# Kernel optimization log

Measured on AMD Instinct MI355X. Metric: run time of the kernel, lower is better.

Reference implementation:

```python
import jax, jax.numpy as jnp
import numpy as np

NEG = -1e30  # log-space 'zero' (safe substitute for -inf)
EPS = 1e-7   # keras.backend.epsilon(), used by ctc_batch_cost


def _ctc_forward(logp, z, allow2):
    """CTC negative log-likelihood via the forward DP in log space.
    logp:   [B, T, C] log-probabilities
    z:      [B, S] extended label sequence (blanks interleaved), S = 2L+1
    allow2: [B, S] bool, whether the skip transition (s-2 -> s) is legal
    Returns [B, 1] loss (matches keras ctc_batch_cost output shape).
    """
    B, T, C = logp.shape
    S = z.shape[1]
    # Gather per-timestep log-probs of extended labels: [B, T, S] -> [T, B, S]
    b_idx = jnp.arange(B)[:, None, None]
    t_idx = jnp.arange(T)[None, :, None]
    lp_z = jnp.transpose(logp[b_idx, t_idx, z[:, None, :]], (1, 0, 2))

    s_idx = jnp.arange(S)[None, :]
    alpha0 = jnp.where(s_idx < 2, lp_z[0], NEG)  # paths may start at blank or first label

    def step(alpha, lp_t):
        a1 = jnp.concatenate([jnp.full((B, 1), NEG, alpha.dtype), alpha[:, :-1]], axis=1)
        a2 = jnp.concatenate([jnp.full((B, 2), NEG, alpha.dtype), alpha[:, :-2]], axis=1)
        a2 = jnp.where(allow2, a2, NEG)
        m = jnp.maximum(alpha, jnp.maximum(a1, a2))
        lse = m + jnp.log(jnp.exp(alpha - m) + jnp.exp(a1 - m) + jnp.exp(a2 - m))
        return lp_t + lse, None

    alphaT, _ = jax.lax.scan(step, alpha0, lp_z[1:])
    # Paths end at last blank (S-1) or last label (S-2)
    last, last2 = alphaT[:, -1], alphaT[:, -2]
    m = jnp.maximum(last, last2)
    ll = m + jnp.log(jnp.exp(last - m) + jnp.exp(last2 - m))
    return -ll[:, None]


def setup_inputs() -> dict:
    key = jax.random.key(0)
    k1, k2 = jax.random.split(key)
    B, T, C, L = 32, 2048, 256, 256
    # ctc_batch_cost expects post-softmax probabilities
    y_pred = jax.nn.softmax(jax.random.normal(k1, (B, T, C), jnp.float32), axis=-1)
    y_true = jax.random.randint(k2, (B, L), 0, C - 1)  # blank = C-1 excluded from labels
    return {"y_true": y_true, "y_pred": y_pred}


def reference(y_true, y_pred):
    B, T, C = y_pred.shape
    blank = C - 1
    L = y_true.shape[1]
    S = 2 * L + 1
    labels = y_true.astype(jnp.int32)
    # Extended label sequence: blank, l0, blank, l1, ..., blank
    z = jnp.full((B, S), blank, jnp.int32).at[:, 1::2].set(labels)
    z_m2 = jnp.concatenate([jnp.full((B, 2), -1, jnp.int32), z[:, :-2]], axis=1)
    allow2 = (z != blank) & (z != z_m2)
    logp = jnp.log(y_pred + EPS)
    return _ctc_forward(logp, z, allow2)
```

## Files before the change

kernel.cpp:

```cpp
#include <hip/hip_runtime.h>

#define TT   2048
#define CC   256
#define LL   256
#define SS   513
#define TM   1023
#define EPSF (1e-7f)
#define LN2F (0.69314718055994531f)
#define DPTH 8
#define RBTH 64
#define NCH  127
#define EMINI (-2000000000)

#if __has_builtin(__builtin_amdgcn_frexp_expf)
#define FREXP_EXP __builtin_amdgcn_frexp_expf
#else
static __device__ __forceinline__ int FREXP_EXP(float x){ int e; frexpf(x,&e); return e; }
#endif
#if __has_builtin(__builtin_amdgcn_ldexpf)
#define LDEXP __builtin_amdgcn_ldexpf
#else
#define LDEXP ldexpf
#endif


__launch_bounds__(128, 1)
__global__ void ctc_mim_kernel(const int* __restrict__ y_true,
                               const float* __restrict__ y_pred,
                               float* __restrict__ out)
{
    __shared__ float cw[SS];
    __shared__ int   ew[64];

    const int tid   = threadIdx.x;
    const int w     = tid >> 6;
    const int lane  = tid & 63;
    const int b     = blockIdx.x;
    const int blank = CC - 1;

    const int*   lab  = y_true + b * LL;
    const float* base = y_pred + (size_t)b * TT * CC;

    int   col[4];
    float kup[4];
    float kdn[4];
    #pragma unroll
    for (int i = 0; i < 4; ++i) {
        const int li = 4 * lane + i;
        const int z  = lab[li];
        col[i] = z;
        const int zm = (li >= 1) ? lab[li - 1] : -1;
        kup[i] = (z != zm) ? 1.0f : 0.0f;
        kdn[i] = (li <= 254 && lab[li + 1] != z) ? 1.0f : 0.0f;
    }

    float f[9];
    #pragma unroll
    for (int j = 0; j < 9; ++j) f[j] = 0.0f;
    int  e = 0;
    bool lzero;

    if (w == 0) {
        if (lane == 0) {
            f[0] = base[blank]  + EPSF;
            f[1] = base[col[0]] + EPSF;
        }
        lzero = (lane != 0);
    } else {
        if (lane == 63) {
            const float* rT = base + (size_t)(TT - 1) * CC;
            f[7] = rT[col[3]] + EPSF;
            f[8] = rT[blank]  + EPSF;
        }
        lzero = (lane != 63);
    }

    float pfb[DPTH];
    float pfl[DPTH][4];
    #pragma unroll
    for (int k = 0; k < DPTH; ++k) {
        const int r = (w == 0) ? (1 + k) : (TT - 2 - k);
        const float* rp = base + (size_t)r * CC;
        pfb[k] = rp[blank];
        #pragma unroll
        for (int i = 0; i < 4; ++i) pfl[k][i] = rp[col[i]];
    }

    auto renorm = [&]() {
        float m = fmaxf(fmaxf(fmaxf(f[0], f[1]), fmaxf(f[2], f[3])),
                        fmaxf(fmaxf(f[4], f[5]), fmaxf(f[6], fmaxf(f[7], f[8]))));
        const int em = FREXP_EXP(m);
        #pragma unroll
        for (int j = 0; j < 9; ++j) f[j] = LDEXP(f[j], -em);
        e += em;
    };

    auto fwd_step = [&](float pb, float p0, float p1, float p2, float p3) {
        float u7 = __shfl_up(f[7], 1);
        int   ue = __shfl_up(e, 1);
        if (lane == 0) { u7 = 0.0f; ue = e; }
        int dlt = ue - e;
        const bool rb = lzero || (dlt >= RBTH);
        if (__ballot(rb)) {
            const int sh = rb ? -dlt : 0;
            #pragma unroll
            for (int j = 0; j < 9; ++j) f[j] = LDEXP(f[j], sh);
            e   = rb ? ue : e;
            dlt = rb ? 0  : dlt;
            lzero = lzero && (u7 == 0.0f);
        }
        const float bf = LDEXP(u7, dlt);
        const float n0 = (f[0] + bf) * pb;
        const float n1 = (f[1] + f[0] + bf   * kup[0]) * p0;
        const float n2 = (f[2] + f[1]) * pb;
        const float n3 = (f[3] + f[2] + f[1] * kup[1]) * p1;
        const float n4 = (f[4] + f[3]) * pb;
        const float n5 = (f[5] + f[4] + f[3] * kup[2]) * p2;
        const float n6 = (f[6] + f[5]) * pb;
        const float n7 = (f[7] + f[6] + f[5] * kup[3]) * p3;
        const float n8 = (f[8] + f[7]) * pb;
        f[0]=n0; f[1]=n1; f[2]=n2; f[3]=n3; f[4]=n4;
        f[5]=n5; f[6]=n6; f[7]=n7; f[8]=n8;
    };

    auto bwd_step = [&](float pb, float p0, float p1, float p2, float p3) {
        float d1 = __shfl_down(f[1], 1);
        int   de = __shfl_down(e, 1);
        if (lane == 63) { d1 = 0.0f; de = e; }
        int dlt = de - e;
        const bool rb = lzero || (dlt >= RBTH);
        if (__ballot(rb)) {
            const int sh = rb ? -dlt : 0;
            #pragma unroll
            for (int j = 0; j < 9; ++j) f[j] = LDEXP(f[j], sh);
            e   = rb ? de : e;
            dlt = rb ? 0  : dlt;
            lzero = lzero && (d1 == 0.0f);
        }
        const float bf = LDEXP(d1, dlt);
        const float n0 = (f[0] + f[1]) * pb;
        const float n1 = (f[1] + f[2] + f[3] * kdn[0]) * p0;
        const float n2 = (f[2] + f[3]) * pb;
        const float n3 = (f[3] + f[4] + f[5] * kdn[1]) * p1;
        const float n4 = (f[4] + f[5]) * pb;
        const float n5 = (f[5] + f[6] + f[7] * kdn[2]) * p2;
        const float n6 = (f[6] + f[7]) * pb;
        const float n7 = (f[7] + f[8] + bf   * kdn[3]) * p3;
        const float n8 = (f[8] + bf) * pb;
        f[0]=n0; f[1]=n1; f[2]=n2; f[3]=n3; f[4]=n4;
        f[5]=n5; f[6]=n6; f[7]=n7; f[8]=n8;
    };

    if (w == 0) {
        for (int c = 0; c < NCH; ++c) {
            #pragma unroll
            for (int k = 0; k < DPTH; ++k) {
                const float pb = pfb[k]    + EPSF;
                const float p0 = pfl[k][0] + EPSF;
                const float p1 = pfl[k][1] + EPSF;
                const float p2 = pfl[k][2] + EPSF;
                const float p3 = pfl[k][3] + EPSF;
                int tp = 1 + c * DPTH + k + DPTH; if (tp > TM) tp = TM;
                const float* rp = base + (size_t)tp * CC;
                pfb[k] = rp[blank];
                #pragma unroll
                for (int i = 0; i < 4; ++i) pfl[k][i] = rp[col[i]];
                fwd_step(pb, p0, p1, p2, p3);
                if (k == 3 || k == 7) renorm();
            }
        }
        #pragma unroll
        for (int k = 0; k < 7; ++k) {
            fwd_step(pfb[k] + EPSF, pfl[k][0] + EPSF, pfl[k][1] + EPSF,
                     pfl[k][2] + EPSF, pfl[k][3] + EPSF);
            if (k == 3) renorm();
        }
    } else {
        for (int c = 0; c < NCH; ++c) {
            #pragma unroll
            for (int k = 0; k < DPTH; ++k) {
                const float pb = pfb[k]    + EPSF;
                const float p0 = pfl[k][0] + EPSF;
                const float p1 = pfl[k][1] + EPSF;
                const float p2 = pfl[k][2] + EPSF;
                const float p3 = pfl[k][3] + EPSF;
                int tp = (TT - 2) - (c * DPTH + k) - DPTH; if (tp < TM + 1) tp = TM + 1;
                const float* rp = base + (size_t)tp * CC;
                pfb[k] = rp[blank];
                #pragma unroll
                for (int i = 0; i < 4; ++i) pfl[k][i] = rp[col[i]];
                bwd_step(pb, p0, p1, p2, p3);
                if (k == 3 || k == 7) renorm();
            }
        }
        #pragma unroll
        for (int k = 0; k < 7; ++k) {
            bwd_step(pfb[k] + EPSF, pfl[k][0] + EPSF, pfl[k][1] + EPSF,
                     pfl[k][2] + EPSF, pfl[k][3] + EPSF);
            if (k == 3) renorm();
        }

        float d1 = __shfl_down(f[1], 1);
        int   de = __shfl_down(e, 1);
        if (lane == 63) { d1 = 0.0f; de = e; }
        int dlt = de - e;
        if (dlt >= RBTH) {
            #pragma unroll
            for (int j = 0; j < 9; ++j) f[j] = LDEXP(f[j], -dlt);
            e = de; dlt = 0;
        }
        const float bf = LDEXP(d1, dlt);
        float cb[9];
        cb[0] = f[0] + f[1];
        cb[1] = f[1] + f[2] + f[3] * kdn[0];
        cb[2] = f[2] + f[3];
        cb[3] = f[3] + f[4] + f[5] * kdn[1];
        cb[4] = f[4] + f[5];
        cb[5] = f[5] + f[6] + f[7] * kdn[2];
        cb[6] = f[6] + f[7];
        cb[7] = f[7] + f[8] + bf   * kdn[3];
        cb[8] = f[8] + bf;

        #pragma unroll
        for (int j = 0; j < 8; ++j) cw[8 * lane + j] = cb[j];
        if (lane == 63) cw[512] = cb[8];
        ew[lane] = e;
    }

    __syncthreads();

    if (w == 0) {
        float part = 0.0f;
        #pragma unroll
        for (int j = 0; j < 8; ++j) part += f[j] * cw[8 * lane + j];
        if (lane == 63) part += f[8] * cw[512];
        int   ep = (part > 0.0f) ? (e + ew[lane]) : EMINI;
        float m  = part;
        #pragma unroll
        for (int d = 1; d < 64; d <<= 1) {
            const float mo = __shfl_xor(m, d);
            const int   eo = __shfl_xor(ep, d);
            const int   E  = max(ep, eo);
            m  = LDEXP(m, ep - E) + LDEXP(mo, eo - E);
            ep = E;
        }
        if (lane == 0)
            out[b] = -LN2F * ((float)ep + __builtin_amdgcn_logf(m));
    }
}

extern "C" void kernel_launch(void* const* d_in, const int* in_sizes, int n_in,
                              void* d_out, int out_size, void* d_ws, size_t ws_size,
                              hipStream_t stream)
{
    const int*   y_true = (const int*)d_in[0];
    const float* y_pred = (const float*)d_in[1];
    float*       out    = (float*)d_out;
    const int B = in_sizes[0] / LL;
    ctc_mim_kernel<<<B, 128, 0, stream>>>(y_true, y_pred, out);
}
```

Baseline: 195.7 us.

## Stage probability rows into an LDS ring via async global-to-LDS loads

Replaces the per-lane scattered global gathers of five probabilities per timestep with coalesced 16-byte-per-lane global_load_lds copies of whole rows into a 10-slot shared-memory ring. The five values are then read from LDS and double-buffered in registers, with explicit vmcnt waits keeping 8 rows in flight. The goal is to hide global latency on the serial DP chain and avoid uncoalesced gathers. The cost is more LDS traffic, a dependence on hand-written waitcnt ordering without an explicit LDS fence, and a rewritten loop tail.

Result: slower. 286.5 us (+46.4%).

```diff
diff --git a/kernel.cpp b/kernel.cpp
--- a/kernel.cpp
+++ b/kernel.cpp
@@ -7,9 +7,9 @@
 #define TM   1023
 #define EPSF (1e-7f)
 #define LN2F (0.69314718055994531f)
-#define DPTH 8
+#define RING 10
+#define RD   8
 #define RBTH 64
-#define NCH  127
 #define EMINI (-2000000000)
 
 #if __has_builtin(__builtin_amdgcn_frexp_expf)
@@ -23,12 +23,21 @@
 #define LDEXP ldexpf
 #endif
 
+__device__ __forceinline__ void stage16(const float* g, float* l)
+{
+    __builtin_amdgcn_global_load_lds(
+        (const __attribute__((address_space(1))) unsigned int*)g,
+        (__attribute__((address_space(3))) unsigned int*)l,
+        16, 0, 0);
+}
+
 
 __launch_bounds__(128, 1)
 __global__ void ctc_mim_kernel(const int* __restrict__ y_true,
                                const float* __restrict__ y_pred,
                                float* __restrict__ out)
 {
+    __shared__ float ring[2][RING][CC];
     __shared__ float cw[SS];
     __shared__ int   ew[64];
 
@@ -73,17 +82,6 @@
             f[8] = rT[blank]  + EPSF;
         }
         lzero = (lane != 63);
-    }
-
-    float pfb[DPTH];
-    float pfl[DPTH][4];
-    #pragma unroll
-    for (int k = 0; k < DPTH; ++k) {
-        const int r = (w == 0) ? (1 + k) : (TT - 2 - k);
-        const float* rp = base + (size_t)r * CC;
-        pfb[k] = rp[blank];
-        #pragma unroll
-        for (int i = 0; i < 4; ++i) pfl[k][i] = rp[col[i]];
     }
 
     auto renorm = [&]() {
@@ -151,53 +149,80 @@
         f[5]=n5; f[6]=n6; f[7]=n7; f[8]=n8;
     };
 
+#define LDPV(PV, SLOT) do {                                   \
+        PV[0] = ring[w][(SLOT)][col[0]] + EPSF;               \
+        PV[1] = ring[w][(SLOT)][col[1]] + EPSF;               \
+        PV[2] = ring[w][(SLOT)][col[2]] + EPSF;               \
+        PV[3] = ring[w][(SLOT)][col[3]] + EPSF;               \
+        PV[4] = ring[w][(SLOT)][CC - 1] + EPSF;               \
+    } while (0)
+
+#define VMWAIT(N) do {                                        \
+        asm volatile("s_waitcnt vmcnt(" #N ")" ::: "memory"); \
+        __builtin_amdgcn_sched_barrier(0);                    \
+    } while (0)
+
+    float pvA[5], pvB[5];
+
+    #pragma unroll
+    for (int j = 0; j < RD; ++j) {
+        const int r = (w == 0) ? (1 + j) : (TT - 2 - j);
+        stage16(base + (size_t)r * CC + 4 * lane, &ring[w][j][0]);
+    }
+    VMWAIT(7);
+    LDPV(pvA, 0);
+
     if (w == 0) {
-        for (int c = 0; c < NCH; ++c) {
-            #pragma unroll
-            for (int k = 0; k < DPTH; ++k) {
-                const float pb = pfb[k]    + EPSF;
-                const float p0 = pfl[k][0] + EPSF;
-                const float p1 = pfl[k][1] + EPSF;
-                const float p2 = pfl[k][2] + EPSF;
-                const float p3 = pfl[k][3] + EPSF;
-                int tp = 1 + c * DPTH + k + DPTH; if (tp > TM) tp = TM;
-                const float* rp = base + (size_t)tp * CC;
-                pfb[k] = rp[blank];
-                #pragma unroll
-                for (int i = 0; i < 4; ++i) pfl[k][i] = rp[col[i]];
-                fwd_step(pb, p0, p1, p2, p3);
+        for (int c = 0; c < 102; ++c) {
+            const int tb = 1 + c * 10;
+            #pragma unroll
+            for (int k = 0; k < 10; ++k) {
+                VMWAIT(6);
+                if ((k & 1) == 0) LDPV(pvB, (k + 1) % RING);
+                else              LDPV(pvA, (k + 1) % RING);
+                int sr = tb + k + RD; if (sr > TM) sr = TM;
+                stage16(base + (size_t)sr * CC + 4 * lane,
+                        &ring[w][(k + RD) % RING][0]);
+                if ((k & 1) == 0) fwd_step(pvA[4], pvA[0], pvA[1], pvA[2], pvA[3]);
+                else              fwd_step(pvB[4], pvB[0], pvB[1], pvB[2], pvB[3]);
                 if (k == 3 || k == 7) renorm();
             }
         }
         #pragma unroll
-        for (int k = 0; k < 7; ++k) {
-            fwd_step(pfb[k] + EPSF, pfl[k][0] + EPSF, pfl[k][1] + EPSF,
-                     pfl[k][2] + EPSF, pfl[k][3] + EPSF);
-            if (k == 3) renorm();
+        for (int k = 0; k < 3; ++k) {
+            VMWAIT(6);
+            if ((k & 1) == 0) LDPV(pvB, (k + 1) % RING);
+            else              LDPV(pvA, (k + 1) % RING);
+            stage16(base + (size_t)TM * CC + 4 * lane,
+                    &ring[w][(k + RD) % RING][0]);
+            if ((k & 1) == 0) fwd_step(pvA[4], pvA[0], pvA[1], pvA[2], pvA[3]);
+            else              fwd_step(pvB[4], pvB[0], pvB[1], pvB[2], pvB[3]);
         }
     } else {
-        for (int c = 0; c < NCH; ++c) {
-            #pragma unroll
-            for (int k = 0; k < DPTH; ++k) {
-                const float pb = pfb[k]    + EPSF;
-                const float p0 = pfl[k][0] + EPSF;
-                const float p1 = pfl[k][1] + EPSF;
-                const float p2 = pfl[k][2] + EPSF;
-                const float p3 = pfl[k][3] + EPSF;
-                int tp = (TT - 2) - (c * DPTH + k) - DPTH; if (tp < TM + 1) tp = TM + 1;
-                const float* rp = base + (size_t)tp * CC;
-                pfb[k] = rp[blank];
-                #pragma unroll
-                for (int i = 0; i < 4; ++i) pfl[k][i] = rp[col[i]];
-                bwd_step(pb, p0, p1, p2, p3);
+        for (int c = 0; c < 102; ++c) {
+            const int ib = c * 10;
+            #pragma unroll
+            for (int k = 0; k < 10; ++k) {
+                VMWAIT(6);
+                if ((k & 1) == 0) LDPV(pvB, (k + 1) % RING);
+                else              LDPV(pvA, (k + 1) % RING);
+                int sr = (TT - 2) - (ib + k + RD); if (sr < TM + 1) sr = TM + 1;
+                stage16(base + (size_t)sr * CC + 4 * lane,
+                        &ring[w][(k + RD) % RING][0]);
+                if ((k & 1) == 0) bwd_step(pvA[4], pvA[0], pvA[1], pvA[2], pvA[3]);
+                else              bwd_step(pvB[4], pvB[0], pvB[1], pvB[2], pvB[3]);
                 if (k == 3 || k == 7) renorm();
             }
         }
         #pragma unroll
-        for (int k = 0; k < 7; ++k) {
-            bwd_step(pfb[k] + EPSF, pfl[k][0] + EPSF, pfl[k][1] + EPSF,
-                     pfl[k][2] + EPSF, pfl[k][3] + EPSF);
-            if (k == 3) renorm();
+        for (int k = 0; k < 3; ++k) {
+            VMWAIT(6);
+            if ((k & 1) == 0) LDPV(pvB, (k + 1) % RING);
+            else              LDPV(pvA, (k + 1) % RING);
+            stage16(base + (size_t)(TM + 1) * CC + 4 * lane,
+                    &ring[w][(k + RD) % RING][0]);
+            if ((k & 1) == 0) bwd_step(pvA[4], pvA[0], pvA[1], pvA[2], pvA[3]);
+            else              bwd_step(pvB[4], pvB[0], pvB[1], pvB[2], pvB[3]);
         }
 
         float d1 = __shfl_down(f[1], 1);
```

## Pre-gather label probabilities into compact workspace before the recurrence kernel

Applied to the files above, without the earlier changes.

A separate, highly parallel kernel gathers per-timestep probabilities of each label and of the blank, with epsilon already added, into a contiguous workspace row of stride 260. The serial forward/backward kernel then reads one float4 plus one scalar per lane per step, replacing five scattered gathers. This is meant to take random-access gather latency off the latency-bound recurrence. The cost is an extra launch and writing then re-reading about 67MB of workspace. A fallback kernel identical to the old code runs when the workspace is too small.

Measured after the change: 205.1 us. 4.8% more time.

```diff
diff --git a/kernel.cpp b/kernel.cpp
--- a/kernel.cpp
+++ b/kernel.cpp
@@ -11,11 +11,12 @@
 #define RBTH 64
 #define NCH  127
 #define EMINI (-2000000000)
+#define GSTR 260
 
 #if __has_builtin(__builtin_amdgcn_frexp_expf)
 #define FREXP_EXP __builtin_amdgcn_frexp_expf
 #else
-static __device__ __forceinline__ int FREXP_EXP(float x){ int e; frexpf(x,&e); return e; }
+static __device__ __forceinline__ int FREXP_EXP(float x){ int e; return (frexpf(x,&e), e); }
 #endif
 #if __has_builtin(__builtin_amdgcn_ldexpf)
 #define LDEXP __builtin_amdgcn_ldexpf
@@ -23,11 +24,31 @@
 #define LDEXP ldexpf
 #endif
 
+__launch_bounds__(256, 4)
+__global__ void ctc_gather_kernel(const int* __restrict__ y_true,
+                                  const float* __restrict__ y_pred,
+                                  float* __restrict__ gat)
+{
+    const int b   = blockIdx.x;
+    const int i   = threadIdx.x;
+    const int col = y_true[b * LL + i];
+    const float* rp = y_pred + (size_t)b * TT * CC;
+    float*       gp = gat    + (size_t)b * TT * GSTR;
+    const int tch = TT / gridDim.y;
+    const int t0  = blockIdx.y * tch;
+    #pragma unroll 4
+    for (int t = t0; t < t0 + tch; ++t) {
+        gp[(size_t)t * GSTR + i] = rp[(size_t)t * CC + col] + EPSF;
+        if (i == 255)
+            gp[(size_t)t * GSTR + 256] = rp[(size_t)t * CC + (CC - 1)] + EPSF;
+    }
+}
 
 __launch_bounds__(128, 1)
-__global__ void ctc_mim_kernel(const int* __restrict__ y_true,
-                               const float* __restrict__ y_pred,
-                               float* __restrict__ out)
+__global__ void ctc_fast_kernel(const int* __restrict__ y_true,
+                                const float* __restrict__ y_pred,
+                                const float* __restrict__ gat,
+                                float* __restrict__ out)
 {
     __shared__ float cw[SS];
     __shared__ int   ew[64];
@@ -38,17 +59,17 @@
     const int b     = blockIdx.x;
     const int blank = CC - 1;
 
-    const int*   lab  = y_true + b * LL;
-    const float* base = y_pred + (size_t)b * TT * CC;
-
-    int   col[4];
+    const int*   lab   = y_true + b * LL;
+    const float* base  = y_pred + (size_t)b * TT * CC;
+    const float* gbase = gat    + (size_t)b * TT * GSTR;
+
+    int   col0 = lab[4 * lane];
     float kup[4];
     float kdn[4];
     #pragma unroll
     for (int i = 0; i < 4; ++i) {
         const int li = 4 * lane + i;
         const int z  = lab[li];
-        col[i] = z;
         const int zm = (li >= 1) ? lab[li - 1] : -1;
         kup[i] = (z != zm) ? 1.0f : 0.0f;
         kdn[i] = (li <= 254 && lab[li + 1] != z) ? 1.0f : 0.0f;
@@ -62,28 +83,27 @@
 
     if (w == 0) {
         if (lane == 0) {
-            f[0] = base[blank]  + EPSF;
-            f[1] = base[col[0]] + EPSF;
+            f[0] = base[blank] + EPSF;
+            f[1] = base[col0]  + EPSF;
         }
         lzero = (lane != 0);
     } else {
         if (lane == 63) {
             const float* rT = base + (size_t)(TT - 1) * CC;
-            f[7] = rT[col[3]] + EPSF;
-            f[8] = rT[blank]  + EPSF;
+            f[7] = rT[lab[255]] + EPSF;
+            f[8] = rT[blank]    + EPSF;
         }
         lzero = (lane != 63);
     }
 
-    float pfb[DPTH];
-    float pfl[DPTH][4];
+    float4 pf[DPTH];
+    float  pbf[DPTH];
     #pragma unroll
     for (int k = 0; k < DPTH; ++k) {
         const int r = (w == 0) ? (1 + k) : (TT - 2 - k);
-        const float* rp = base + (size_t)r * CC;
-        pfb[k] = rp[blank];
-        #pragma unroll
-        for (int i = 0; i < 4; ++i) pfl[k][i] = rp[col[i]];
+        const float* rp = gbase + (size_t)r * GSTR;
+        pf[k]  = *(const float4*)(rp + 4 * lane);
+        pbf[k] = rp[256];
     }
 
     auto renorm = [&]() {
@@ -155,48 +175,41 @@
         for (int c = 0; c < NCH; ++c) {
             #pragma unroll
             for (int k = 0; k < DPTH; ++k) {
-                const float pb = pfb[k]    + EPSF;
-                const float p0 = pfl[k][0] + EPSF;
-                const float p1 = pfl[k][1] + EPSF;
-                const float p2 = pfl[k][2] + EPSF;
-                const float p3 = pfl[k][3] + EPSF;
+                const float pb = pbf[k];
+                const float p0 = pf[k].x, p1 = pf[k].y,
+                            p2 = pf[k].z, p3 = pf[k].w;
                 int tp = 1 + c * DPTH + k + DPTH; if (tp > TM) tp = TM;
-                const float* rp = base + (size_t)tp * CC;
-                pfb[k] = rp[blank];
-                #pragma unroll
-                for (int i = 0; i < 4; ++i) pfl[k][i] = rp[col[i]];
+                const float* rp = gbase + (size_t)tp * GSTR;
+                pf[k]  = *(const float4*)(rp + 4 * lane);
+                pbf[k] = rp[256];
                 fwd_step(pb, p0, p1, p2, p3);
                 if (k == 3 || k == 7) renorm();
             }
         }
         #pragma unroll
         for (int k = 0; k < 7; ++k) {
-            fwd_step(pfb[k] + EPSF, pfl[k][0] + EPSF, pfl[k][1] + EPSF,
-                     pfl[k][2] + EPSF, pfl[k][3] + EPSF);
+            fwd_step(pbf[k], pf[k].x, pf[k].y, pf[k].z, pf[k].w);
             if (k == 3) renorm();
         }
     } else {
         for (int c = 0; c < NCH; ++c) {
             #pragma unroll
             for (int k = 0; k < DPTH; ++k) {
-                const float pb = pfb[k]    + EPSF;
-                const float p0 = pfl[k][0] + EPSF;
-                const float p1 = pfl[k][1] + EPSF;
-                const float p2 = pfl[k][2] + EPSF;
-                const float p3 = pfl[k][3] + EPSF;
-                int tp = (TT - 2) - (c * DPTH + k) - DPTH; if (tp < TM + 1) tp = TM + 1;
-                const float* rp = base + (size_t)tp * CC;
-                pfb[k] = rp[blank];
-                #pragma unroll
-                for (int i = 0; i < 4; ++i) pfl[k][i] = rp[col[i]];
+                const float pb = pbf[k];
+                const float p0 = pf[k].x, p1 = pf[k].y,
+                            p2 = pf[k].z, p3 = pf[k].w;
+                int tp = (TT - 2) - (c * DPTH + k) - DPTH;
+                if (tp < TM + 1) tp = TM + 1;
+                const float* rp = gbase + (size_t)tp * GSTR;
+                pf[k]  = *(const float4*)(rp + 4 * lane);
+                pbf[k] = rp[256];
                 bwd_step(pb, p0, p1, p2, p3);
                 if (k == 3 || k == 7) renorm();
             }
         }
         #pragma unroll
         for (int k = 0; k < 7; ++k) {
-            bwd_step(pfb[k] + EPSF, pfl[k][0] + EPSF, pfl[k][1] + EPSF,
-                     pfl[k][2] + EPSF, pfl[k][3] + EPSF);
+            bwd_step(pbf[k], pf[k].x, pf[k].y, pf[k].z, pf[k].w);
             if (k == 3) renorm();
         }
 
@@ -240,7 +253,217 @@
         for (int d = 1; d < 64; d <<= 1) {
             const float mo = __shfl_xor(m, d);
             const int   eo = __shfl_xor(ep, d);
-            const int   E  = max(ep, eo);
+            const int   E  = ep > eo ? ep : eo;
+            m  = LDEXP(m, ep - E) + LDEXP(mo, eo - E);
+            ep = E;
+        }
+        if (lane == 0)
+            out[b] = -LN2F * ((float)ep + __builtin_amdgcn_logf(m));
+    }
+}
+
+__launch_bounds__(128, 1)
+__global__ void ctc_fb_kernel(const int* __restrict__ y_true,
+                              const float* __restrict__ y_pred,
+                              float* __restrict__ out)
+{
+    __shared__ float cw[SS];
+    __shared__ int   ew[64];
+
+    const int tid   = threadIdx.x;
+    const int w     = tid >> 6;
+    const int lane  = tid & 63;
+    const int b     = blockIdx.x;
+    const int blank = CC - 1;
+
+    const int*   lab  = y_true + b * LL;
+    const float* base = y_pred + (size_t)b * TT * CC;
+
+    int   col[4];
+    float kup[4], kdn[4];
+    #pragma unroll
+    for (int i = 0; i < 4; ++i) {
+        const int li = 4 * lane + i;
+        const int z  = lab[li];
+        col[i] = z;
+        const int zm = (li >= 1) ? lab[li - 1] : -1;
+        kup[i] = (z != zm) ? 1.0f : 0.0f;
+        kdn[i] = (li <= 254 && lab[li + 1] != z) ? 1.0f : 0.0f;
+    }
+
+    float f[9];
+    #pragma unroll
+    for (int j = 0; j < 9; ++j) f[j] = 0.0f;
+    int  e = 0;
+    bool lzero;
+
+    if (w == 0) {
+        if (lane == 0) { f[0] = base[blank] + EPSF; f[1] = base[col[0]] + EPSF; }
+        lzero = (lane != 0);
+    } else {
+        if (lane == 63) {
+            const float* rT = base + (size_t)(TT - 1) * CC;
+            f[7] = rT[col[3]] + EPSF; f[8] = rT[blank] + EPSF;
+        }
+        lzero = (lane != 63);
+    }
+
+    float pfb[DPTH]; float pfl[DPTH][4];
+    #pragma unroll
+    for (int k = 0; k < DPTH; ++k) {
+        const int r = (w == 0) ? (1 + k) : (TT - 2 - k);
+        const float* rp = base + (size_t)r * CC;
+        pfb[k] = rp[blank];
+        #pragma unroll
+        for (int i = 0; i < 4; ++i) pfl[k][i] = rp[col[i]];
+    }
+
+    auto renorm = [&]() {
+        float m = fmaxf(fmaxf(fmaxf(f[0], f[1]), fmaxf(f[2], f[3])),
+                        fmaxf(fmaxf(f[4], f[5]), fmaxf(f[6], fmaxf(f[7], f[8]))));
+        const int em = FREXP_EXP(m);
+        #pragma unroll
+        for (int j = 0; j < 9; ++j) f[j] = LDEXP(f[j], -em);
+        e += em;
+    };
+    auto fwd_step = [&](float pb, float p0, float p1, float p2, float p3) {
+        float u7 = __shfl_up(f[7], 1);
+        int   ue = __shfl_up(e, 1);
+        if (lane == 0) { u7 = 0.0f; ue = e; }
+        int dlt = ue - e;
+        const bool rb = lzero || (dlt >= RBTH);
+        if (__ballot(rb)) {
+            const int sh = rb ? -dlt : 0;
+            #pragma unroll
+            for (int j = 0; j < 9; ++j) f[j] = LDEXP(f[j], sh);
+            e = rb ? ue : e; dlt = rb ? 0 : dlt;
+            lzero = lzero && (u7 == 0.0f);
+        }
+        const float bf = LDEXP(u7, dlt);
+        const float n0 = (f[0] + bf) * pb;
+        const float n1 = (f[1] + f[0] + bf   * kup[0]) * p0;
+        const float n2 = (f[2] + f[1]) * pb;
+        const float n3 = (f[3] + f[2] + f[1] * kup[1]) * p1;
+        const float n4 = (f[4] + f[3]) * pb;
+        const float n5 = (f[5] + f[4] + f[3] * kup[2]) * p2;
+        const float n6 = (f[6] + f[5]) * pb;
+        const float n7 = (f[7] + f[6] + f[5] * kup[3]) * p3;
+        const float n8 = (f[8] + f[7]) * pb;
+        f[0]=n0; f[1]=n1; f[2]=n2; f[3]=n3; f[4]=n4;
+        f[5]=n5; f[6]=n6; f[7]=n7; f[8]=n8;
+    };
+    auto bwd_step = [&](float pb, float p0, float p1, float p2, float p3) {
+        float d1 = __shfl_down(f[1], 1);
+        int   de = __shfl_down(e, 1);
+        if (lane == 63) { d1 = 0.0f; de = e; }
+        int dlt = de - e;
+        const bool rb = lzero || (dlt >= RBTH);
+        if (__ballot(rb)) {
+            const int sh = rb ? -dlt : 0;
+            #pragma unroll
+            for (int j = 0; j < 9; ++j) f[j] = LDEXP(f[j], sh);
+            e = rb ? de : e; dlt = rb ? 0 : dlt;
+            lzero = lzero && (d1 == 0.0f);
+        }
+        const float bf = LDEXP(d1, dlt);
+        const float n0 = (f[0] + f[1]) * pb;
+        const float n1 = (f[1] + f[2] + f[3] * kdn[0]) * p0;
+        const float n2 = (f[2] + f[3]) * pb;
+        const float n3 = (f[3] + f[4] + f[5] * kdn[1]) * p1;
+        const float n4 = (f[4] + f[5]) * pb;
+        const float n5 = (f[5] + f[6] + f[7] * kdn[2]) * p2;
+        const float n6 = (f[6] + f[7]) * pb;
+        const float n7 = (f[7] + f[8] + bf   * kdn[3]) * p3;
+        const float n8 = (f[8] + bf) * pb;
+        f[0]=n0; f[1]=n1; f[2]=n2; f[3]=n3; f[4]=n4;
+        f[5]=n5; f[6]=n6; f[7]=n7; f[8]=n8;
+    };
+
+    if (w == 0) {
+        for (int c = 0; c < NCH; ++c) {
+            #pragma unroll
+            for (int k = 0; k < DPTH; ++k) {
+                const float pb = pfb[k] + EPSF;
+                const float p0 = pfl[k][0] + EPSF, p1 = pfl[k][1] + EPSF;
+                const float p2 = pfl[k][2] + EPSF, p3 = pfl[k][3] + EPSF;
+                int tp = 1 + c * DPTH + k + DPTH; if (tp > TM) tp = TM;
+                const float* rp = base + (size_t)tp * CC;
+                pfb[k] = rp[blank];
+                #pragma unroll
+                for (int i = 0; i < 4; ++i) pfl[k][i] = rp[col[i]];
+                fwd_step(pb, p0, p1, p2, p3);
+                if (k == 3 || k == 7) renorm();
+            }
+        }
+        #pragma unroll
+        for (int k = 0; k < 7; ++k) {
+            fwd_step(pfb[k] + EPSF, pfl[k][0] + EPSF, pfl[k][1] + EPSF,
+                     pfl[k][2] + EPSF, pfl[k][3] + EPSF);
+            if (k == 3) renorm();
+        }
+    } else {
+        for (int c = 0; c < NCH; ++c) {
+            #pragma unroll
+            for (int k = 0; k < DPTH; ++k) {
+                const float pb = pfb[k] + EPSF;
+                const float p0 = pfl[k][0] + EPSF, p1 = pfl[k][1] + EPSF;
+                const float p2 = pfl[k][2] + EPSF, p3 = pfl[k][3] + EPSF;
+                int tp = (TT - 2) - (c * DPTH + k) - DPTH; if (tp < TM + 1) tp = TM + 1;
+                const float* rp = base + (size_t)tp * CC;
+                pfb[k] = rp[blank];
+                #pragma unroll
+                for (int i = 0; i < 4; ++i) pfl[k][i] = rp[col[i]];
+                bwd_step(pb, p0, p1, p2, p3);
+                if (k == 3 || k == 7) renorm();
+            }
+        }
+        #pragma unroll
+        for (int k = 0; k < 7; ++k) {
+            bwd_step(pfb[k] + EPSF, pfl[k][0] + EPSF, pfl[k][1] + EPSF,
+                     pfl[k][2] + EPSF, pfl[k][3] + EPSF);
+            if (k == 3) renorm();
+        }
+
+        float d1 = __shfl_down(f[1], 1);
+        int   de = __shfl_down(e, 1);
+        if (lane == 63) { d1 = 0.0f; de = e; }
+        int dlt = de - e;
+        if (dlt >= RBTH) {
+            #pragma unroll
+            for (int j = 0; j < 9; ++j) f[j] = LDEXP(f[j], -dlt);
+            e = de; dlt = 0;
+        }
+        const float bf = LDEXP(d1, dlt);
+        float cb[9];
+        cb[0] = f[0] + f[1];
+        cb[1] = f[1] + f[2] + f[3] * kdn[0];
+        cb[2] = f[2] + f[3];
+        cb[3] = f[3] + f[4] + f[5] * kdn[1];
+        cb[4] = f[4] + f[5];
+        cb[5] = f[5] + f[6] + f[7] * kdn[2];
+        cb[6] = f[6] + f[7];
+        cb[7] = f[7] + f[8] + bf   * kdn[3];
+        cb[8] = f[8] + bf;
+        #pragma unroll
+        for (int j = 0; j < 8; ++j) cw[8 * lane + j] = cb[j];
+        if (lane == 63) cw[512] = cb[8];
+        ew[lane] = e;
+    }
+
+    __syncthreads();
+
+    if (w == 0) {
+        float part = 0.0f;
+        #pragma unroll
+        for (int j = 0; j < 8; ++j) part += f[j] * cw[8 * lane + j];
+        if (lane == 63) part += f[8] * cw[512];
+        int   ep = (part > 0.0f) ? (e + ew[lane]) : EMINI;
+        float m  = part;
+        #pragma unroll
+        for (int d = 1; d < 64; d <<= 1) {
+            const float mo = __shfl_xor(m, d);
+            const int   eo = __shfl_xor(ep, d);
+            const int   E  = ep > eo ? ep : eo;
             m  = LDEXP(m, ep - E) + LDEXP(mo, eo - E);
             ep = E;
         }
@@ -257,5 +480,13 @@
     const float* y_pred = (const float*)d_in[1];
     float*       out    = (float*)d_out;
     const int B = in_sizes[0] / LL;
-    ctc_mim_kernel<<<B, 128, 0, stream>>>(y_true, y_pred, out);
+
+    const size_t need = (size_t)B * TT * GSTR * sizeof(float);
+    if (ws_size >= need) {
+        float* gat = (float*)d_ws;
+        ctc_gather_kernel<<<dim3(B, 32), 256, 0, stream>>>(y_true, y_pred, gat);
+        ctc_fast_kernel<<<B, 128, 0, stream>>>(y_true, y_pred, gat, out);
+    } else {
+        ctc_fb_kernel<<<B, 128, 0, stream>>>(y_true, y_pred, out);
+    }
 }
```
